# Optimization experiments

Hardware: AMD Instinct MI355X
Metric: run time of the kernel (lower is better)

## Reference

```python
import jax, jax.numpy as jnp
import numpy as np

FT = 0.2  # clip floor (init arg ft)

def _norm_mat(m):
    # matrix / (count of nonzeros along last dim + 1e-30)
    deg = jnp.sum(m != 0, axis=-1, keepdims=True).astype(m.dtype)
    return m / (deg + 1e-30)

def _l2n(x):
    return x / (jnp.linalg.norm(x, axis=-1, keepdims=True) + 1e-30)

def setup_inputs():
    B, L, D, H, O = 2, 2048, 64, 64, 128
    N = 2 * L
    ks = jax.random.split(jax.random.key(0), 30)
    u = lambda i, s: jax.random.uniform(ks[i], s, jnp.float32)
    g = lambda i, s: jax.random.normal(ks[i], s, jnp.float32) * 0.05
    inp = {}
    inp['word_outputs_0'] = g(0, (B, L, D))
    inp['word_outputs_1'] = g(1, (B, L, D))
    inp['node_hidden'] = g(2, (B, D))
    inp['op_embedding'] = g(3, (B, O, D))
    inp['word_exist_sequence'] = (u(4, (B, N)) < 0.8).astype(jnp.float32)
    inp['word_exist_matrix'] = (u(5, (B, N, N)) < 0.8).astype(jnp.float32)
    inp['word_operator'] = (u(6, (B, N, O)) < 0.02).astype(jnp.float32)
    inp['word_word'] = (u(7, (B, N, N)) < 0.01).astype(jnp.float32)
    inp['depend_0'] = (u(8, (B, L, L)) < 0.05).astype(jnp.float32)
    inp['depend_1'] = (u(9, (B, L, L)) < 0.05).astype(jnp.float32)
    inp['goal_word'] = u(10, (B, N))
    names = [('Wg', (D, H)), ('bg', (H,)), ('Wwk', (D, H)), ('bwk', (H,)),
             ('Wws', (D, H)), ('bws', (H,)), ('Wo', (D, D)), ('bo', (D,)),
             ('Wupd', (3 * H, D)), ('bupd', (D,)), ('Wf', (3 * H + D, D)), ('bf', (D,)),
             ('Wf2', (2 * D, D)), ('bf2', (D,)), ('Wout', (D, D)), ('bout', (D,))]
    for i, (nm, s) in enumerate(names):
        inp[nm] = g(11 + i, s)
    return inp

def _forward(w0, w1, nh, opE, wes, wem, wop, ww, d0, d1, gw,
             Wg, bg, Wwk, bwk, Wws, bws, Wo, bo, Wupd, bupd, Wf, bf, Wf2, bf2, Wout, bout):
    all_w = jnp.concatenate([w0, w1], axis=1)                      # [B,N,D]
    goal_trans = (nh @ Wg + bg)[:, None, :]                        # [B,1,H] (broadcast = expand)
    word_g = _l2n(goal_trans * gw[..., None])                      # [B,N,H]
    word_w_k = _l2n(jnp.matmul(_norm_mat(ww * wem), all_w @ Wwk + bwk))
    ws0 = jnp.matmul(_norm_mat(d0), w0 @ Wws + bws)
    ws1 = jnp.matmul(_norm_mat(d1), w1 @ Wws + bws)
    word_w_s = _l2n(jnp.concatenate([ws0, ws1], axis=1))           # [B,N,H]
    neigh = jnp.concatenate([word_g, word_w_k, word_w_s], axis=-1)  # [B,N,3H]
    forget = jax.nn.sigmoid(jnp.concatenate([all_w, word_g, word_w_k, word_w_s], axis=-1) @ Wf + bf)
    word_updated = jnp.maximum(forget, FT) * all_w + (1.0 - forget) * jax.nn.relu(neigh @ Wupd + bupd)
    adj_op = _norm_mat(jnp.swapaxes(wes[..., None] * wop, 1, 2))   # [B,O,N]
    word_op = jnp.matmul(adj_op, word_updated @ Wo + bo)           # [B,O,D]
    forget2 = jax.nn.sigmoid(jnp.concatenate([opE, word_op], axis=-1) @ Wf2 + bf2)
    op_out = jnp.maximum(forget2, FT) * opE + (1.0 - forget2) * jax.nn.relu(word_op @ Wout + bout)
    # original returns (split(word_updated), op_embedding); concat along node axis here
    return jnp.concatenate([word_updated, op_out], axis=1)         # [B,N+O,D]

def reference(word_outputs_0, word_outputs_1, node_hidden, op_embedding,
              word_exist_sequence, word_exist_matrix, word_operator, word_word,
              depend_0, depend_1, goal_word,
              Wg, bg, Wwk, bwk, Wws, bws, Wo, bo, Wupd, bupd, Wf, bf, Wf2, bf2, Wout, bout):
    return _forward(word_outputs_0, word_outputs_1, node_hidden, op_embedding,
                    word_exist_sequence, word_exist_matrix, word_operator, word_word,
                    depend_0, depend_1, goal_word,
                    Wg, bg, Wwk, bwk, Wws, bws, Wo, bo, Wupd, bupd, Wf, bf, Wf2, bf2, Wout, bout)
```

## Files before the change

### kernel.cpp

```cpp
#include <hip/hip_runtime.h>
#include <cstdint>

typedef unsigned short u16;
typedef unsigned long long u64;

__device__ __forceinline__ u16 f2b(float f){
  union { float f; uint32_t i; } v; v.f = f;
  uint32_t r = v.i + 0x7FFFu + ((v.i >> 16) & 1u);
  return (u16)(r >> 16);
}
__device__ __forceinline__ float b2f(u16 u){
  union { uint32_t i; float f; } v; v.i = ((uint32_t)u) << 16; return v.f;
}
__device__ __forceinline__ float sigmoidf(float x){ return 1.0f / (1.0f + __expf(-x)); }

__device__ __forceinline__ void gl_lds4(const void* g, void* l){
  __builtin_amdgcn_global_load_lds((const __attribute__((address_space(1))) void*)g,
                                   (__attribute__((address_space(3))) void*)l, 4, 0, 0);
}
#define WAIT_VM0() __builtin_amdgcn_s_waitcnt(0x0F70)

__global__ __launch_bounds__(256) void k_xform(
    const float* __restrict__ w0, const float* __restrict__ w1,
    const float* __restrict__ Wwk, const float* __restrict__ bwk,
    const float* __restrict__ Wws, const float* __restrict__ bws,
    const float* __restrict__ nh, const float* __restrict__ Wg, const float* __restrict__ bg,
    const float* __restrict__ Wf, const float* __restrict__ Wupd, const float* __restrict__ Wo,
    float* __restrict__ Xk, float* __restrict__ Xs,
    float* __restrict__ ghat, uint32_t* __restrict__ pkWf,
    uint32_t* __restrict__ pkWu, uint32_t* __restrict__ pkWo){
  int tid = threadIdx.x;
  if (blockIdx.x >= 512){
    int aux = blockIdx.x - 512;
    if (aux == 16){
      if (tid < 128){
        int b = tid >> 6, h = tid & 63;
        float g = bg[h];
        for (int d = 0; d < 64; ++d) g += nh[b*64 + d] * Wg[d*64 + h];
        float ss = g * g;
        #pragma unroll
        for (int o = 32; o > 0; o >>= 1) ss += __shfl_xor(ss, o, 64);
        ghat[b*64 + h] = g / (sqrtf(ss) + 1e-30f);
      }
      return;
    }
    for (int k = tid; k < 1024; k += 256){
      int i = aux*1024 + k;
      const float* src; uint32_t* dst; int li;
      if (i < 8192){ src = Wf; dst = pkWf; li = i; }
      else if (i < 14336){ src = Wupd; dst = pkWu; li = i - 8192; }
      else { src = Wo; dst = pkWo; li = i - 14336; }
      int k2 = li >> 6, ln = li & 63;
      dst[li] = (uint32_t)f2b(src[(2*k2)*64 + ln]) | ((uint32_t)f2b(src[(2*k2+1)*64 + ln]) << 16);
    }
    return;
  }
  __shared__ float sWk[4096], sWs[4096];
  for (int i = tid; i < 1024; i += 256){
    ((float4*)sWk)[i] = ((const float4*)Wwk)[i];
    ((float4*)sWs)[i] = ((const float4*)Wws)[i];
  }
  __syncthreads();
  int lane = tid & 63, wave = tid >> 6;
  float bk = bwk[lane], bs = bws[lane];
  float aw[4];
  #pragma unroll
  for (int t = 0; t < 4; ++t){
    int row = blockIdx.x*4 + wave + t*2048;
    int b = row >> 12, n = row & 4095;
    aw[t] = (n < 2048) ? w0[((size_t)(b*2048 + n))*64 + lane]
                       : w1[((size_t)(b*2048 + n - 2048))*64 + lane];
  }
  #pragma unroll
  for (int t = 0; t < 4; ++t){
    int row = blockIdx.x*4 + wave + t*2048;
    float xk = bk, xs = bs;
    #pragma unroll 8
    for (int d = 0; d < 64; ++d){
      float a = __shfl(aw[t], d, 64);
      xk += a * sWk[d*64 + lane];
      xs += a * sWs[d*64 + lane];
    }
    Xk[(size_t)row*64 + lane] = xk;
    Xs[(size_t)row*64 + lane] = xs;
  }
}

__global__ __launch_bounds__(256) void k_bits_all(
    const float* __restrict__ ww, const float* __restrict__ wem,
    const float* __restrict__ d0, const float* __restrict__ d1,
    const float* __restrict__ wes, const float* __restrict__ wop,
    u64* __restrict__ bitBig, u64* __restrict__ bitD0, u64* __restrict__ bitD1,
    u64* __restrict__ bitOp){
  int wid = blockIdx.x*4 + (threadIdx.x >> 6);
  int lane = threadIdx.x & 63;
  if (wid >= 49152){
    int ng0 = (wid - 49152) * 8;
    #pragma unroll
    for (int i = 0; i < 8; ++i){
      int n = ng0 + i;
      float vx = wop[(size_t)n*128 + lane];
      float vy = wop[(size_t)n*128 + 64 + lane];
      float e  = wes[n];
      u64 m0 = __ballot((e != 0.f) && (vx != 0.f));
      u64 m1 = __ballot((e != 0.f) && (vy != 0.f));
      if (lane == 0) bitOp[(size_t)n*2]     = m0;
      if (lane == 1) bitOp[(size_t)n*2 + 1] = m1;
    }
    return;
  }
  const float *A, *B; u64* dst;
  if (wid < 32768){
    A = ww + (size_t)wid*1024; B = wem + (size_t)wid*1024; dst = bitBig + (size_t)wid*16;
  } else if (wid < 40960){
    size_t c = wid - 32768; A = d0 + c*1024; B = A; dst = bitD0 + c*16;
  } else {
    size_t c = wid - 40960; A = d1 + c*1024; B = A; dst = bitD1 + c*16;
  }
  const float4* ap = (const float4*)A + lane;
  const float4* bp = (const float4*)B + lane;
  float4 a0 = ap[0], a1 = ap[64], a2 = ap[128], a3 = ap[192];
  float4 b0 = bp[0], b1 = bp[64], b2 = bp[128], b3 = bp[192];
  u64 myw = 0;
#define B4(i, va, vb) { \
  u64 m0 = __ballot((va.x != 0.f) && (vb.x != 0.f)); \
  u64 m1 = __ballot((va.y != 0.f) && (vb.y != 0.f)); \
  u64 m2 = __ballot((va.z != 0.f) && (vb.z != 0.f)); \
  u64 m3 = __ballot((va.w != 0.f) && (vb.w != 0.f)); \
  if (lane == (i)*4 + 0) myw = m0; \
  if (lane == (i)*4 + 1) myw = m1; \
  if (lane == (i)*4 + 2) myw = m2; \
  if (lane == (i)*4 + 3) myw = m3; }
  B4(0, a0, b0) B4(1, a1, b1) B4(2, a2, b2) B4(3, a3, b3)
#undef B4
  if (lane < 16) dst[lane] = myw;
}

__global__ __launch_bounds__(256) void k_gath_all(
    const u64* __restrict__ bitBig, const u64* __restrict__ bitD0, const u64* __restrict__ bitD1,
    const float* __restrict__ Xk, const float* __restrict__ Xs,
    u16* __restrict__ wwkn, u16* __restrict__ wwsn){
  __shared__ int q[4][256];
  __shared__ float rows[4][16][64];
  int lane = threadIdx.x & 63, wave = threadIdx.x >> 6;
  int wid = blockIdx.x*4 + wave;
  const u64* bits; const float* XbBase; u16* op; int WPR;
  if (wid < 8192){
    WPR = 64; bits = bitBig + (size_t)wid*64;
    int b = wid >> 12;
    XbBase = Xk + (size_t)b*4096*64;
    op = wwkn + (size_t)wid*64;
  } else if (wid < 12288){
    int lr = wid - 8192; WPR = 32; bits = bitD0 + (size_t)lr*32;
    int b = lr >> 11, r = lr & 2047;
    XbBase = Xs + (size_t)b*4096*64;
    op = wwsn + ((size_t)b*4096 + r)*64;
  } else {
    int lr = wid - 12288; WPR = 32; bits = bitD1 + (size_t)lr*32;
    int b = lr >> 11, r = lr & 2047;
    XbBase = Xs + ((size_t)b*4096 + 2048)*64;
    op = wwsn + ((size_t)b*4096 + 2048 + r)*64;
  }
  u64 word = (lane < WPR) ? bits[lane] : 0ULL;
  int c = __popcll(word);
  int pre = c;
  #pragma unroll
  for (int off = 1; off < 64; off <<= 1){
    int t = __shfl_up(pre, off, 64);
    if (lane >= off) pre += t;
  }
  int total = __shfl(pre, 63, 64);
  int base = pre - c;
  int colhi = (lane >> 2) * 256 + (lane & 3);
  u64 m = word;
  while (m){
    int p = __builtin_ctzll(m); m &= m - 1;
    q[wave][base++] = colhi + p*4;
  }
  float acc = 0.f;
  int i = 0;
  for (; i + 16 <= total; i += 16){
    int4 c0 = *(const int4*)&q[wave][i];
    int4 c1 = *(const int4*)&q[wave][i + 4];
    int4 c2 = *(const int4*)&q[wave][i + 8];
    int4 c3 = *(const int4*)&q[wave][i + 12];
    gl_lds4(XbBase + (size_t)c0.x*64 + lane, &rows[wave][ 0][0]);
    gl_lds4(XbBase + (size_t)c0.y*64 + lane, &rows[wave][ 1][0]);
    gl_lds4(XbBase + (size_t)c0.z*64 + lane, &rows[wave][ 2][0]);
    gl_lds4(XbBase + (size_t)c0.w*64 + lane, &rows[wave][ 3][0]);
    gl_lds4(XbBase + (size_t)c1.x*64 + lane, &rows[wave][ 4][0]);
    gl_lds4(XbBase + (size_t)c1.y*64 + lane, &rows[wave][ 5][0]);
    gl_lds4(XbBase + (size_t)c1.z*64 + lane, &rows[wave][ 6][0]);
    gl_lds4(XbBase + (size_t)c1.w*64 + lane, &rows[wave][ 7][0]);
    gl_lds4(XbBase + (size_t)c2.x*64 + lane, &rows[wave][ 8][0]);
    gl_lds4(XbBase + (size_t)c2.y*64 + lane, &rows[wave][ 9][0]);
    gl_lds4(XbBase + (size_t)c2.z*64 + lane, &rows[wave][10][0]);
    gl_lds4(XbBase + (size_t)c2.w*64 + lane, &rows[wave][11][0]);
    gl_lds4(XbBase + (size_t)c3.x*64 + lane, &rows[wave][12][0]);
    gl_lds4(XbBase + (size_t)c3.y*64 + lane, &rows[wave][13][0]);
    gl_lds4(XbBase + (size_t)c3.z*64 + lane, &rows[wave][14][0]);
    gl_lds4(XbBase + (size_t)c3.w*64 + lane, &rows[wave][15][0]);
    WAIT_VM0();
    float s0 = 0.f, s1 = 0.f, s2 = 0.f, s3 = 0.f;
    #pragma unroll
    for (int r = 0; r < 4; ++r){
      s0 += rows[wave][r][lane];
      s1 += rows[wave][4 + r][lane];
      s2 += rows[wave][8 + r][lane];
      s3 += rows[wave][12 + r][lane];
    }
    acc += (s0 + s1) + (s2 + s3);
  }
  for (; i < total; ++i) acc += XbBase[(size_t)q[wave][i]*64 + lane];
  float ss = acc * acc;
  #pragma unroll
  for (int o = 32; o > 0; o >>= 1) ss += __shfl_xor(ss, o, 64);
  op[lane] = f2b(acc / (sqrtf(ss) + 1e-30f));
}

__global__ __launch_bounds__(256, 2) void k_update(
    const float* __restrict__ w0, const float* __restrict__ w1,
    const float* __restrict__ gw, const float* __restrict__ ghat,
    const u16* __restrict__ wwkn, const u16* __restrict__ wwsn,
    const uint32_t* __restrict__ pkWf, const uint32_t* __restrict__ pkWu,
    const uint32_t* __restrict__ pkWo,
    const float* __restrict__ bf, const float* __restrict__ bupd, const float* __restrict__ bo,
    float* __restrict__ out, float* __restrict__ WUo){
  __shared__ uint32_t pWf[8192];
  __shared__ uint32_t pWu[6144];
  __shared__ uint32_t pWo[2048];
  __shared__ float xsh[4][256];
  int tid = threadIdx.x;
  for (int i = tid; i < 2048; i += 256) ((uint4*)pWf)[i] = ((const uint4*)pkWf)[i];
  for (int i = tid; i < 1536; i += 256) ((uint4*)pWu)[i] = ((const uint4*)pkWu)[i];
  for (int i = tid; i < 512;  i += 256) ((uint4*)pWo)[i] = ((const uint4*)pkWo)[i];
  __syncthreads();
  int lane = tid & 63, wave = tid >> 6;
  float bff = bf[lane], bup = bupd[lane], boo = bo[lane];
  float aw[4], wgv[4], wk[4], wsv[4];
  #pragma unroll
  for (int t = 0; t < 4; ++t){
    int row = blockIdx.x*4 + wave + t*2048;
    int b = row >> 12, n = row & 4095;
    aw[t] = (n < 2048) ? w0[((size_t)(b*2048 + n))*64 + lane]
                       : w1[((size_t)(b*2048 + n - 2048))*64 + lane];
    float gvv = gw[b*4096 + n];
    wgv[t] = (gvv != 0.f) ? ghat[b*64 + lane] : 0.f;
    wk[t]  = b2f(wwkn[(size_t)row*64 + lane]);
    wsv[t] = b2f(wwsn[(size_t)row*64 + lane]);
  }
  #pragma unroll
  for (int t = 0; t < 4; ++t){
    int row = blockIdx.x*4 + wave + t*2048;
    int b = row >> 12, n = row & 4095;
    xsh[wave][lane] = aw[t]; xsh[wave][64 + lane] = wgv[t];
    xsh[wave][128 + lane] = wk[t]; xsh[wave][192 + lane] = wsv[t];
    float f = bff, u = bup;
    #pragma unroll 8
    for (int k2 = 0; k2 < 32; ++k2){
      float2 xv = *(const float2*)&xsh[wave][2*k2];
      uint32_t wf = pWf[k2*64 + lane];
      f += xv.x * b2f((u16)wf) + xv.y * b2f((u16)(wf >> 16));
    }
    #pragma unroll 8
    for (int k2 = 32; k2 < 128; ++k2){
      float2 xv = *(const float2*)&xsh[wave][2*k2];
      uint32_t wf = pWf[k2*64 + lane];
      uint32_t wu = pWu[(k2 - 32)*64 + lane];
      f += xv.x * b2f((u16)wf) + xv.y * b2f((u16)(wf >> 16));
      u += xv.x * b2f((u16)wu) + xv.y * b2f((u16)(wu >> 16));
    }
    f = sigmoidf(f);
    u = fmaxf(u, 0.f);
    float wu = fmaxf(f, 0.2f) * aw[t] + (1.f - f) * u;
    out[((size_t)b*4224 + n)*64 + lane] = wu;
    float o = boo;
    #pragma unroll 8
    for (int k2 = 0; k2 < 32; ++k2){
      uint32_t wo2 = pWo[k2*64 + lane];
      o += __shfl(wu, 2*k2, 64) * b2f((u16)wo2) + __shfl(wu, 2*k2 + 1, 64) * b2f((u16)(wo2 >> 16));
    }
    WUo[(size_t)row*64 + lane] = o;
  }
}

__global__ __launch_bounds__(256) void k_opfin(
    const u64* __restrict__ bitOp, const float* __restrict__ WUo,
    const float* __restrict__ opE,
    const float* __restrict__ Wf2, const float* __restrict__ bf2,
    const float* __restrict__ Wout, const float* __restrict__ bout,
    float* __restrict__ out){
  __shared__ float sW2[8192];
  __shared__ float sWo[4096];
  __shared__ int q[4][96];
  __shared__ float sacc[4][64];
  __shared__ int scnt[4];
  __shared__ float xsh[128];
  int tid = threadIdx.x, lane = tid & 63, wave = tid >> 6;
  for (int i = tid; i < 2048; i += 256) ((float4*)sW2)[i] = ((const float4*)Wf2)[i];
  for (int i = tid; i < 1024; i += 256) ((float4*)sWo)[i] = ((const float4*)Wout)[i];
  int rowIdx = blockIdx.x;
  int b = rowIdx >> 7, o = rowIdx & 127;
  int wrd = o >> 6, bit = o & 63;
  const u64* bp = bitOp + (size_t)b*8192 + (size_t)wave*2048 + wrd;
  u64 lt = (1ULL << lane) - 1ULL;
  u64 vv[16];
  #pragma unroll
  for (int it = 0; it < 16; ++it) vv[it] = bp[(size_t)(it*64 + lane)*2];
  int cnt = 0;
  #pragma unroll
  for (int it = 0; it < 16; ++it){
    bool nz = (vv[it] >> bit) & 1ULL;
    u64 m = __ballot(nz);
    if (nz) q[wave][cnt + (int)__popcll(m & lt)] = wave*1024 + it*64 + lane;
    cnt += (int)__popcll(m);
  }
  const float* Xb = WUo + (size_t)b*4096*64 + lane;
  float acc = 0.f;
  int i = 0;
  for (; i + 8 <= cnt; i += 8){
    int4 c0 = *(const int4*)&q[wave][i];
    int4 c1 = *(const int4*)&q[wave][i + 4];
    float v0 = Xb[(size_t)c0.x*64], v1 = Xb[(size_t)c0.y*64];
    float v2 = Xb[(size_t)c0.z*64], v3 = Xb[(size_t)c0.w*64];
    float v4 = Xb[(size_t)c1.x*64], v5 = Xb[(size_t)c1.y*64];
    float v6 = Xb[(size_t)c1.z*64], v7 = Xb[(size_t)c1.w*64];
    acc += ((v0 + v1) + (v2 + v3)) + ((v4 + v5) + (v6 + v7));
  }
  for (; i < cnt; ++i) acc += Xb[(size_t)q[wave][i]*64];
  sacc[wave][lane] = acc;
  if (lane == 0) scnt[wave] = cnt;
  __syncthreads();
  if (wave == 0){
    float t = sacc[0][lane] + sacc[1][lane] + sacc[2][lane] + sacc[3][lane];
    float deg = (float)(scnt[0] + scnt[1] + scnt[2] + scnt[3]);
    float wo = t / (deg + 1e-30f);
    float e  = opE[(size_t)rowIdx*64 + lane];
    xsh[lane] = e; xsh[64 + lane] = wo;
    float f = bf2[lane], u = bout[lane];
    #pragma unroll 8
    for (int k = 0; k < 128; ++k) f += xsh[k] * sW2[k*64 + lane];
    #pragma unroll 8
    for (int d = 0; d < 64; ++d)  u += xsh[64 + d] * sWo[d*64 + lane];
    f = sigmoidf(f);
    u = fmaxf(u, 0.f);
    float res = fmaxf(f, 0.2f) * e + (1.f - f) * u;
    out[((size_t)b*4224 + 4096 + o)*64 + lane] = res;
  }
}

extern "C" void kernel_launch(void* const* d_in, const int* in_sizes, int n_in,
                              void* d_out, int out_size, void* d_ws, size_t ws_size,
                              hipStream_t stream){
  const float* w0   = (const float*)d_in[0];
  const float* w1   = (const float*)d_in[1];
  const float* nh   = (const float*)d_in[2];
  const float* opE  = (const float*)d_in[3];
  const float* wes  = (const float*)d_in[4];
  const float* wem  = (const float*)d_in[5];
  const float* wop  = (const float*)d_in[6];
  const float* ww   = (const float*)d_in[7];
  const float* d0   = (const float*)d_in[8];
  const float* d1   = (const float*)d_in[9];
  const float* gw   = (const float*)d_in[10];
  const float* Wg   = (const float*)d_in[11];
  const float* bg   = (const float*)d_in[12];
  const float* Wwk  = (const float*)d_in[13];
  const float* bwk  = (const float*)d_in[14];
  const float* Wws  = (const float*)d_in[15];
  const float* bws  = (const float*)d_in[16];
  const float* Wo   = (const float*)d_in[17];
  const float* bo   = (const float*)d_in[18];
  const float* Wupd = (const float*)d_in[19];
  const float* bupd = (const float*)d_in[20];
  const float* Wf   = (const float*)d_in[21];
  const float* bf   = (const float*)d_in[22];
  const float* Wf2  = (const float*)d_in[23];
  const float* bf2  = (const float*)d_in[24];
  const float* Wout = (const float*)d_in[25];
  const float* bout = (const float*)d_in[26];

  float* ws    = (float*)d_ws;
  float* ghat  = ws;
  float* Xk    = ws + 128;
  float* Xs    = ws + 524416;
  uint32_t* pkWf = (uint32_t*)(ws + 1048704);
  uint32_t* pkWu = (uint32_t*)(ws + 1056896);
  uint32_t* pkWo = (uint32_t*)(ws + 1063040);
  u64*  bitBig = (u64*)(ws + 1065088);
  u64*  bitD0  = (u64*)(ws + 2113664);
  u64*  bitD1  = (u64*)(ws + 2375808);
  u64*  bitOp  = (u64*)(ws + 2637952);
  u16*  wwkn   = (u16*)(ws + 2670720);
  u16*  wwsn   = (u16*)(ws + 2932864);
  float* WUo   = Xs;
  float* out   = (float*)d_out;

  k_xform<<<529, 256, 0, stream>>>(w0, w1, Wwk, bwk, Wws, bws, nh, Wg, bg,
                                   Wf, Wupd, Wo, Xk, Xs, ghat, pkWf, pkWu, pkWo);
  k_bits_all<<<12544, 256, 0, stream>>>(ww, wem, d0, d1, wes, wop,
                                        bitBig, bitD0, bitD1, bitOp);
  k_gath_all<<<4096, 256, 0, stream>>>(bitBig, bitD0, bitD1, Xk, Xs, wwkn, wwsn);
  k_update<<<512, 256, 0, stream>>>(w0, w1, gw, ghat, wwkn, wwsn,
                                    pkWf, pkWu, pkWo, bf, bupd, bo, out, WUo);
  k_opfin<<<256, 256, 0, stream>>>(bitOp, WUo, opE, Wf2, bf2, Wout, bout, out);
}
```

Baseline: 447.5 us.

## Aggregate raw word rows before linear projection and drop separate transform kernel

Uses linearity: instead of projecting every word through Wwk/Wws and then gathering projected rows, the gather kernel sums raw w0/w1 rows over each sparse neighbour set, then applies the 64x64 weight once per row, adding count times bias. This removes the k_xform kernel and its intermediate Xk/Xs buffers, and the weight packing and goal setup are folded into the bit-mask kernel as extra blocks. Each gather block now loads both weight matrices into LDS and does a per-row matvec after aggregation, which raises per-block LDS use and work; key and structural gathers run in one wave sequentially.

```diff
diff --git a/kernel.cpp b/kernel.cpp
--- a/kernel.cpp
+++ b/kernel.cpp
@@ -20,18 +20,18 @@
 }
 #define WAIT_VM0() __builtin_amdgcn_s_waitcnt(0x0F70)
 
-__global__ __launch_bounds__(256) void k_xform(
-    const float* __restrict__ w0, const float* __restrict__ w1,
-    const float* __restrict__ Wwk, const float* __restrict__ bwk,
-    const float* __restrict__ Wws, const float* __restrict__ bws,
+__global__ __launch_bounds__(256) void k_bits_all(
+    const float* __restrict__ ww, const float* __restrict__ wem,
+    const float* __restrict__ d0, const float* __restrict__ d1,
+    const float* __restrict__ wes, const float* __restrict__ wop,
     const float* __restrict__ nh, const float* __restrict__ Wg, const float* __restrict__ bg,
     const float* __restrict__ Wf, const float* __restrict__ Wupd, const float* __restrict__ Wo,
-    float* __restrict__ Xk, float* __restrict__ Xs,
-    float* __restrict__ ghat, uint32_t* __restrict__ pkWf,
-    uint32_t* __restrict__ pkWu, uint32_t* __restrict__ pkWo){
+    u64* __restrict__ bitBig, u64* __restrict__ bitD0, u64* __restrict__ bitD1,
+    u64* __restrict__ bitOp, float* __restrict__ ghat,
+    uint32_t* __restrict__ pkWf, uint32_t* __restrict__ pkWu, uint32_t* __restrict__ pkWo){
   int tid = threadIdx.x;
-  if (blockIdx.x >= 512){
-    int aux = blockIdx.x - 512;
+  if (blockIdx.x >= 12544){
+    int aux = blockIdx.x - 12544;
     if (aux == 16){
       if (tid < 128){
         int b = tid >> 6, h = tid & 63;
@@ -55,45 +55,8 @@
     }
     return;
   }
-  __shared__ float sWk[4096], sWs[4096];
-  for (int i = tid; i < 1024; i += 256){
-    ((float4*)sWk)[i] = ((const float4*)Wwk)[i];
-    ((float4*)sWs)[i] = ((const float4*)Wws)[i];
-  }
-  __syncthreads();
-  int lane = tid & 63, wave = tid >> 6;
-  float bk = bwk[lane], bs = bws[lane];
-  float aw[4];
-  #pragma unroll
-  for (int t = 0; t < 4; ++t){
-    int row = blockIdx.x*4 + wave + t*2048;
-    int b = row >> 12, n = row & 4095;
-    aw[t] = (n < 2048) ? w0[((size_t)(b*2048 + n))*64 + lane]
-                       : w1[((size_t)(b*2048 + n - 2048))*64 + lane];
-  }
-  #pragma unroll
-  for (int t = 0; t < 4; ++t){
-    int row = blockIdx.x*4 + wave + t*2048;
-    float xk = bk, xs = bs;
-    #pragma unroll 8
-    for (int d = 0; d < 64; ++d){
-      float a = __shfl(aw[t], d, 64);
-      xk += a * sWk[d*64 + lane];
-      xs += a * sWs[d*64 + lane];
-    }
-    Xk[(size_t)row*64 + lane] = xk;
-    Xs[(size_t)row*64 + lane] = xs;
-  }
-}
-
-__global__ __launch_bounds__(256) void k_bits_all(
-    const float* __restrict__ ww, const float* __restrict__ wem,
-    const float* __restrict__ d0, const float* __restrict__ d1,
-    const float* __restrict__ wes, const float* __restrict__ wop,
-    u64* __restrict__ bitBig, u64* __restrict__ bitD0, u64* __restrict__ bitD1,
-    u64* __restrict__ bitOp){
-  int wid = blockIdx.x*4 + (threadIdx.x >> 6);
-  int lane = threadIdx.x & 63;
+  int wid = blockIdx.x*4 + (tid >> 6);
+  int lane = tid & 63;
   if (wid >= 49152){
     int ng0 = (wid - 49152) * 8;
     #pragma unroll
@@ -136,86 +99,152 @@
   if (lane < 16) dst[lane] = myw;
 }
 
-__global__ __launch_bounds__(256) void k_gath_all(
+__global__ __launch_bounds__(256) void k_gath2(
     const u64* __restrict__ bitBig, const u64* __restrict__ bitD0, const u64* __restrict__ bitD1,
-    const float* __restrict__ Xk, const float* __restrict__ Xs,
+    const float* __restrict__ w0, const float* __restrict__ w1,
+    const float* __restrict__ Wwk, const float* __restrict__ bwk,
+    const float* __restrict__ Wws, const float* __restrict__ bws,
     u16* __restrict__ wwkn, u16* __restrict__ wwsn){
+  __shared__ float sWk[4096], sWs[4096];
   __shared__ int q[4][256];
   __shared__ float rows[4][16][64];
-  int lane = threadIdx.x & 63, wave = threadIdx.x >> 6;
+  int tid = threadIdx.x, lane = tid & 63, wave = tid >> 6;
+  for (int i = tid; i < 1024; i += 256){
+    ((float4*)sWk)[i] = ((const float4*)Wwk)[i];
+    ((float4*)sWs)[i] = ((const float4*)Wws)[i];
+  }
+  __syncthreads();
   int wid = blockIdx.x*4 + wave;
-  const u64* bits; const float* XbBase; u16* op; int WPR;
-  if (wid < 8192){
-    WPR = 64; bits = bitBig + (size_t)wid*64;
-    int b = wid >> 12;
-    XbBase = Xk + (size_t)b*4096*64;
-    op = wwkn + (size_t)wid*64;
-  } else if (wid < 12288){
-    int lr = wid - 8192; WPR = 32; bits = bitD0 + (size_t)lr*32;
-    int b = lr >> 11, r = lr & 2047;
-    XbBase = Xs + (size_t)b*4096*64;
-    op = wwsn + ((size_t)b*4096 + r)*64;
-  } else {
-    int lr = wid - 12288; WPR = 32; bits = bitD1 + (size_t)lr*32;
-    int b = lr >> 11, r = lr & 2047;
-    XbBase = Xs + ((size_t)b*4096 + 2048)*64;
-    op = wwsn + ((size_t)b*4096 + 2048 + r)*64;
-  }
-  u64 word = (lane < WPR) ? bits[lane] : 0ULL;
-  int c = __popcll(word);
-  int pre = c;
-  #pragma unroll
-  for (int off = 1; off < 64; off <<= 1){
-    int t = __shfl_up(pre, off, 64);
-    if (lane >= off) pre += t;
-  }
-  int total = __shfl(pre, 63, 64);
-  int base = pre - c;
-  int colhi = (lane >> 2) * 256 + (lane & 3);
-  u64 m = word;
-  while (m){
-    int p = __builtin_ctzll(m); m &= m - 1;
-    q[wave][base++] = colhi + p*4;
-  }
-  float acc = 0.f;
-  int i = 0;
-  for (; i + 16 <= total; i += 16){
-    int4 c0 = *(const int4*)&q[wave][i];
-    int4 c1 = *(const int4*)&q[wave][i + 4];
-    int4 c2 = *(const int4*)&q[wave][i + 8];
-    int4 c3 = *(const int4*)&q[wave][i + 12];
-    gl_lds4(XbBase + (size_t)c0.x*64 + lane, &rows[wave][ 0][0]);
-    gl_lds4(XbBase + (size_t)c0.y*64 + lane, &rows[wave][ 1][0]);
-    gl_lds4(XbBase + (size_t)c0.z*64 + lane, &rows[wave][ 2][0]);
-    gl_lds4(XbBase + (size_t)c0.w*64 + lane, &rows[wave][ 3][0]);
-    gl_lds4(XbBase + (size_t)c1.x*64 + lane, &rows[wave][ 4][0]);
-    gl_lds4(XbBase + (size_t)c1.y*64 + lane, &rows[wave][ 5][0]);
-    gl_lds4(XbBase + (size_t)c1.z*64 + lane, &rows[wave][ 6][0]);
-    gl_lds4(XbBase + (size_t)c1.w*64 + lane, &rows[wave][ 7][0]);
-    gl_lds4(XbBase + (size_t)c2.x*64 + lane, &rows[wave][ 8][0]);
-    gl_lds4(XbBase + (size_t)c2.y*64 + lane, &rows[wave][ 9][0]);
-    gl_lds4(XbBase + (size_t)c2.z*64 + lane, &rows[wave][10][0]);
-    gl_lds4(XbBase + (size_t)c2.w*64 + lane, &rows[wave][11][0]);
-    gl_lds4(XbBase + (size_t)c3.x*64 + lane, &rows[wave][12][0]);
-    gl_lds4(XbBase + (size_t)c3.y*64 + lane, &rows[wave][13][0]);
-    gl_lds4(XbBase + (size_t)c3.z*64 + lane, &rows[wave][14][0]);
-    gl_lds4(XbBase + (size_t)c3.w*64 + lane, &rows[wave][15][0]);
-    WAIT_VM0();
-    float s0 = 0.f, s1 = 0.f, s2 = 0.f, s3 = 0.f;
+  int b = wid >> 12, n = wid & 4095;
+  const float* w0b = w0 + (size_t)b*131072 + lane;
+  const float* w1b = w1 + (size_t)b*131072 - 131072 + lane;
+
+  {
+    u64 word = bitBig[(size_t)wid*64 + lane];
+    int c = __popcll(word);
+    int pre = c;
     #pragma unroll
-    for (int r = 0; r < 4; ++r){
-      s0 += rows[wave][r][lane];
-      s1 += rows[wave][4 + r][lane];
-      s2 += rows[wave][8 + r][lane];
-      s3 += rows[wave][12 + r][lane];
-    }
-    acc += (s0 + s1) + (s2 + s3);
-  }
-  for (; i < total; ++i) acc += XbBase[(size_t)q[wave][i]*64 + lane];
-  float ss = acc * acc;
-  #pragma unroll
-  for (int o = 32; o > 0; o >>= 1) ss += __shfl_xor(ss, o, 64);
-  op[lane] = f2b(acc / (sqrtf(ss) + 1e-30f));
+    for (int off = 1; off < 64; off <<= 1){
+      int t = __shfl_up(pre, off, 64);
+      if (lane >= off) pre += t;
+    }
+    int total = __shfl(pre, 63, 64);
+    int base = pre - c;
+    int colhi = (lane >> 2) * 256 + (lane & 3);
+    u64 m = word;
+    while (m){
+      int p = __builtin_ctzll(m); m &= m - 1;
+      q[wave][base++] = colhi + p*4;
+    }
+#define GP(j) ((((j) < 2048) ? w0b : w1b) + (size_t)(j)*64)
+    float acc = 0.f;
+    int i = 0;
+    for (; i + 16 <= total; i += 16){
+      int4 c0 = *(const int4*)&q[wave][i];
+      int4 c1 = *(const int4*)&q[wave][i + 4];
+      int4 c2 = *(const int4*)&q[wave][i + 8];
+      int4 c3 = *(const int4*)&q[wave][i + 12];
+      gl_lds4(GP(c0.x), &rows[wave][ 0][0]);
+      gl_lds4(GP(c0.y), &rows[wave][ 1][0]);
+      gl_lds4(GP(c0.z), &rows[wave][ 2][0]);
+      gl_lds4(GP(c0.w), &rows[wave][ 3][0]);
+      gl_lds4(GP(c1.x), &rows[wave][ 4][0]);
+      gl_lds4(GP(c1.y), &rows[wave][ 5][0]);
+      gl_lds4(GP(c1.z), &rows[wave][ 6][0]);
+      gl_lds4(GP(c1.w), &rows[wave][ 7][0]);
+      gl_lds4(GP(c2.x), &rows[wave][ 8][0]);
+      gl_lds4(GP(c2.y), &rows[wave][ 9][0]);
+      gl_lds4(GP(c2.z), &rows[wave][10][0]);
+      gl_lds4(GP(c2.w), &rows[wave][11][0]);
+      gl_lds4(GP(c3.x), &rows[wave][12][0]);
+      gl_lds4(GP(c3.y), &rows[wave][13][0]);
+      gl_lds4(GP(c3.z), &rows[wave][14][0]);
+      gl_lds4(GP(c3.w), &rows[wave][15][0]);
+      WAIT_VM0();
+      float s0 = 0.f, s1 = 0.f, s2 = 0.f, s3 = 0.f;
+      #pragma unroll
+      for (int r = 0; r < 4; ++r){
+        s0 += rows[wave][r][lane];
+        s1 += rows[wave][4 + r][lane];
+        s2 += rows[wave][8 + r][lane];
+        s3 += rows[wave][12 + r][lane];
+      }
+      acc += (s0 + s1) + (s2 + s3);
+    }
+    for (; i < total; ++i) acc += *GP(q[wave][i]);
+#undef GP
+    float y = (float)total * bwk[lane];
+    #pragma unroll 8
+    for (int d = 0; d < 64; ++d) y += __shfl(acc, d, 64) * sWk[d*64 + lane];
+    float ss = y * y;
+    #pragma unroll
+    for (int o = 32; o > 0; o >>= 1) ss += __shfl_xor(ss, o, 64);
+    wwkn[(size_t)wid*64 + lane] = f2b(y / (sqrtf(ss) + 1e-30f));
+  }
+
+  {
+    const u64* bits = (n < 2048) ? (bitD0 + ((size_t)b*2048 + n)*32)
+                                 : (bitD1 + ((size_t)b*2048 + n - 2048)*32);
+    const float* src = ((n < 2048) ? w0 : w1) + (size_t)b*131072 + lane;
+    u64 word = (lane < 32) ? bits[lane] : 0ULL;
+    int c = __popcll(word);
+    int pre = c;
+    #pragma unroll
+    for (int off = 1; off < 64; off <<= 1){
+      int t = __shfl_up(pre, off, 64);
+      if (lane >= off) pre += t;
+    }
+    int total = __shfl(pre, 63, 64);
+    int base = pre - c;
+    int colhi = (lane >> 2) * 256 + (lane & 3);
+    u64 m = word;
+    while (m){
+      int p = __builtin_ctzll(m); m &= m - 1;
+      q[wave][base++] = colhi + p*4;
+    }
+    float acc = 0.f;
+    int i = 0;
+    for (; i + 16 <= total; i += 16){
+      int4 c0 = *(const int4*)&q[wave][i];
+      int4 c1 = *(const int4*)&q[wave][i + 4];
+      int4 c2 = *(const int4*)&q[wave][i + 8];
+      int4 c3 = *(const int4*)&q[wave][i + 12];
+      gl_lds4(src + (size_t)c0.x*64, &rows[wave][ 0][0]);
+      gl_lds4(src + (size_t)c0.y*64, &rows[wave][ 1][0]);
+      gl_lds4(src + (size_t)c0.z*64, &rows[wave][ 2][0]);
+      gl_lds4(src + (size_t)c0.w*64, &rows[wave][ 3][0]);
+      gl_lds4(src + (size_t)c1.x*64, &rows[wave][ 4][0]);
+      gl_lds4(src + (size_t)c1.y*64, &rows[wave][ 5][0]);
+      gl_lds4(src + (size_t)c1.z*64, &rows[wave][ 6][0]);
+      gl_lds4(src + (size_t)c1.w*64, &rows[wave][ 7][0]);
+      gl_lds4(src + (size_t)c2.x*64, &rows[wave][ 8][0]);
+      gl_lds4(src + (size_t)c2.y*64, &rows[wave][ 9][0]);
+      gl_lds4(src + (size_t)c2.z*64, &rows[wave][10][0]);
+      gl_lds4(src + (size_t)c2.w*64, &rows[wave][11][0]);
+      gl_lds4(src + (size_t)c3.x*64, &rows[wave][12][0]);
+      gl_lds4(src + (size_t)c3.y*64, &rows[wave][13][0]);
+      gl_lds4(src + (size_t)c3.z*64, &rows[wave][14][0]);
+      gl_lds4(src + (size_t)c3.w*64, &rows[wave][15][0]);
+      WAIT_VM0();
+      float s0 = 0.f, s1 = 0.f, s2 = 0.f, s3 = 0.f;
+      #pragma unroll
+      for (int r = 0; r < 4; ++r){
+        s0 += rows[wave][r][lane];
+        s1 += rows[wave][4 + r][lane];
+        s2 += rows[wave][8 + r][lane];
+        s3 += rows[wave][12 + r][lane];
+      }
+      acc += (s0 + s1) + (s2 + s3);
+    }
+    for (; i < total; ++i) acc += src[(size_t)q[wave][i]*64];
+    float y = (float)total * bws[lane];
+    #pragma unroll 8
+    for (int d = 0; d < 64; ++d) y += __shfl(acc, d, 64) * sWs[d*64 + lane];
+    float ss = y * y;
+    #pragma unroll
+    for (int o = 32; o > 0; o >>= 1) ss += __shfl_xor(ss, o, 64);
+    wwsn[(size_t)wid*64 + lane] = f2b(y / (sqrtf(ss) + 1e-30f));
+  }
 }
 
 __global__ __launch_bounds__(256, 2) void k_update(
@@ -382,25 +411,23 @@
 
   float* ws    = (float*)d_ws;
   float* ghat  = ws;
-  float* Xk    = ws + 128;
-  float* Xs    = ws + 524416;
-  uint32_t* pkWf = (uint32_t*)(ws + 1048704);
-  uint32_t* pkWu = (uint32_t*)(ws + 1056896);
-  uint32_t* pkWo = (uint32_t*)(ws + 1063040);
-  u64*  bitBig = (u64*)(ws + 1065088);
-  u64*  bitD0  = (u64*)(ws + 2113664);
-  u64*  bitD1  = (u64*)(ws + 2375808);
-  u64*  bitOp  = (u64*)(ws + 2637952);
-  u16*  wwkn   = (u16*)(ws + 2670720);
-  u16*  wwsn   = (u16*)(ws + 2932864);
-  float* WUo   = Xs;
+  uint32_t* pkWf = (uint32_t*)(ws + 128);
+  uint32_t* pkWu = (uint32_t*)(ws + 8320);
+  uint32_t* pkWo = (uint32_t*)(ws + 14464);
+  u64*  bitBig = (u64*)(ws + 16512);
+  u64*  bitD0  = (u64*)(ws + 1065088);
+  u64*  bitD1  = (u64*)(ws + 1327232);
+  u64*  bitOp  = (u64*)(ws + 1589376);
+  u16*  wwkn   = (u16*)(ws + 1622144);
+  u16*  wwsn   = (u16*)(ws + 1884288);
+  float* WUo   = ws + 2146432;
   float* out   = (float*)d_out;
 
-  k_xform<<<529, 256, 0, stream>>>(w0, w1, Wwk, bwk, Wws, bws, nh, Wg, bg,
-                                   Wf, Wupd, Wo, Xk, Xs, ghat, pkWf, pkWu, pkWo);
-  k_bits_all<<<12544, 256, 0, stream>>>(ww, wem, d0, d1, wes, wop,
-                                        bitBig, bitD0, bitD1, bitOp);
-  k_gath_all<<<4096, 256, 0, stream>>>(bitBig, bitD0, bitD1, Xk, Xs, wwkn, wwsn);
+  k_bits_all<<<12561, 256, 0, stream>>>(ww, wem, d0, d1, wes, wop, nh, Wg, bg,
+                                        Wf, Wupd, Wo, bitBig, bitD0, bitD1,
+                                        bitOp, ghat, pkWf, pkWu, pkWo);
+  k_gath2<<<2048, 256, 0, stream>>>(bitBig, bitD0, bitD1, w0, w1,
+                                    Wwk, bwk, Wws, bws, wwkn, wwsn);
   k_update<<<512, 256, 0, stream>>>(w0, w1, gw, ghat, wwkn, wwsn,
                                     pkWf, pkWu, pkWo, bf, bupd, bo, out, WUo);
   k_opfin<<<256, 256, 0, stream>>>(bitOp, WUo, opE, Wf2, bf2, Wout, bout, out);
```

New measurement: 456.7 us. +2.1%, slower.

## Reassociate sparse aggregation to gather raw inputs, apply projection after summing

Applied to the files above, without the earlier changes.

The sparse-adjacency matmul is reordered so each wave builds its nonzero mask and immediately gathers raw w0/w1 rows, producing per-chunk partial sums and counts. The dense Wwk/Wws projection and bias are applied afterwards in a new finishing kernel as S@W + count*b. This removes the separate transform kernel, the bitmask round-trip through memory and one launch. In exchange, partial sums are stored in bf16, which adds rounding before the projection, and row gathers are split across chunks.

```diff
diff --git a/kernel.cpp b/kernel.cpp
--- a/kernel.cpp
+++ b/kernel.cpp
@@ -20,18 +20,22 @@
 }
 #define WAIT_VM0() __builtin_amdgcn_s_waitcnt(0x0F70)
 
-__global__ __launch_bounds__(256) void k_xform(
+__global__ __launch_bounds__(256) void k_bits_all(
+    const float* __restrict__ ww, const float* __restrict__ wem,
+    const float* __restrict__ d0, const float* __restrict__ d1,
+    const float* __restrict__ wes, const float* __restrict__ wop,
     const float* __restrict__ w0, const float* __restrict__ w1,
-    const float* __restrict__ Wwk, const float* __restrict__ bwk,
-    const float* __restrict__ Wws, const float* __restrict__ bws,
     const float* __restrict__ nh, const float* __restrict__ Wg, const float* __restrict__ bg,
     const float* __restrict__ Wf, const float* __restrict__ Wupd, const float* __restrict__ Wo,
-    float* __restrict__ Xk, float* __restrict__ Xs,
-    float* __restrict__ ghat, uint32_t* __restrict__ pkWf,
-    uint32_t* __restrict__ pkWu, uint32_t* __restrict__ pkWo){
+    u16* __restrict__ psumB, int* __restrict__ pcntB,
+    u16* __restrict__ psumD, int* __restrict__ pcntD,
+    u64* __restrict__ bitOp, float* __restrict__ ghat,
+    uint32_t* __restrict__ pkWf, uint32_t* __restrict__ pkWu, uint32_t* __restrict__ pkWo){
+  __shared__ int q[4][256];
+  __shared__ float rows[4][16][64];
   int tid = threadIdx.x;
-  if (blockIdx.x >= 512){
-    int aux = blockIdx.x - 512;
+  if (blockIdx.x >= 12544){
+    int aux = blockIdx.x - 12544;
     if (aux == 16){
       if (tid < 128){
         int b = tid >> 6, h = tid & 63;
@@ -55,45 +59,8 @@
     }
     return;
   }
-  __shared__ float sWk[4096], sWs[4096];
-  for (int i = tid; i < 1024; i += 256){
-    ((float4*)sWk)[i] = ((const float4*)Wwk)[i];
-    ((float4*)sWs)[i] = ((const float4*)Wws)[i];
-  }
-  __syncthreads();
-  int lane = tid & 63, wave = tid >> 6;
-  float bk = bwk[lane], bs = bws[lane];
-  float aw[4];
-  #pragma unroll
-  for (int t = 0; t < 4; ++t){
-    int row = blockIdx.x*4 + wave + t*2048;
-    int b = row >> 12, n = row & 4095;
-    aw[t] = (n < 2048) ? w0[((size_t)(b*2048 + n))*64 + lane]
-                       : w1[((size_t)(b*2048 + n - 2048))*64 + lane];
-  }
-  #pragma unroll
-  for (int t = 0; t < 4; ++t){
-    int row = blockIdx.x*4 + wave + t*2048;
-    float xk = bk, xs = bs;
-    #pragma unroll 8
-    for (int d = 0; d < 64; ++d){
-      float a = __shfl(aw[t], d, 64);
-      xk += a * sWk[d*64 + lane];
-      xs += a * sWs[d*64 + lane];
-    }
-    Xk[(size_t)row*64 + lane] = xk;
-    Xs[(size_t)row*64 + lane] = xs;
-  }
-}
-
-__global__ __launch_bounds__(256) void k_bits_all(
-    const float* __restrict__ ww, const float* __restrict__ wem,
-    const float* __restrict__ d0, const float* __restrict__ d1,
-    const float* __restrict__ wes, const float* __restrict__ wop,
-    u64* __restrict__ bitBig, u64* __restrict__ bitD0, u64* __restrict__ bitD1,
-    u64* __restrict__ bitOp){
-  int wid = blockIdx.x*4 + (threadIdx.x >> 6);
-  int lane = threadIdx.x & 63;
+  int wave = tid >> 6, lane = tid & 63;
+  int wid = blockIdx.x*4 + wave;
   if (wid >= 49152){
     int ng0 = (wid - 49152) * 8;
     #pragma unroll
@@ -109,13 +76,34 @@
     }
     return;
   }
-  const float *A, *B; u64* dst;
+  const float *A, *B;
+  const float *srcA, *srcB;
+  int jbase, thresh;
+  u16* ps; int* pc;
   if (wid < 32768){
-    A = ww + (size_t)wid*1024; B = wem + (size_t)wid*1024; dst = bitBig + (size_t)wid*16;
-  } else if (wid < 40960){
-    size_t c = wid - 32768; A = d0 + c*1024; B = A; dst = bitD0 + c*16;
+    int row = wid >> 2, chunk = wid & 3;
+    int b = row >> 12;
+    A = ww  + (size_t)row*4096 + chunk*1024;
+    B = wem + (size_t)row*4096 + chunk*1024;
+    srcA = w0 + (size_t)b*131072 + lane;
+    srcB = w1 + (size_t)b*131072 - 131072 + lane;
+    jbase = chunk*1024; thresh = 2048;
+    ps = psumB + (size_t)wid*64; pc = pcntB + wid;
   } else {
-    size_t c = wid - 40960; A = d1 + c*1024; B = A; dst = bitD1 + c*16;
+    int idx = wid - 32768;
+    int rowp = idx >> 1, chunk = idx & 1;
+    if (rowp < 4096){
+      int b = rowp >> 11;
+      A = d0 + (size_t)rowp*2048 + chunk*1024;
+      srcA = w0 + (size_t)b*131072 + lane;
+    } else {
+      int rr = rowp - 4096, b = rr >> 11;
+      A = d1 + (size_t)rr*2048 + chunk*1024;
+      srcA = w1 + (size_t)b*131072 + lane;
+    }
+    B = A; srcB = srcA;
+    jbase = chunk*1024; thresh = 4096;
+    ps = psumD + (size_t)idx*64; pc = pcntD + idx;
   }
   const float4* ap = (const float4*)A + lane;
   const float4* bp = (const float4*)B + lane;
@@ -133,36 +121,7 @@
   if (lane == (i)*4 + 3) myw = m3; }
   B4(0, a0, b0) B4(1, a1, b1) B4(2, a2, b2) B4(3, a3, b3)
 #undef B4
-  if (lane < 16) dst[lane] = myw;
-}
-
-__global__ __launch_bounds__(256) void k_gath_all(
-    const u64* __restrict__ bitBig, const u64* __restrict__ bitD0, const u64* __restrict__ bitD1,
-    const float* __restrict__ Xk, const float* __restrict__ Xs,
-    u16* __restrict__ wwkn, u16* __restrict__ wwsn){
-  __shared__ int q[4][256];
-  __shared__ float rows[4][16][64];
-  int lane = threadIdx.x & 63, wave = threadIdx.x >> 6;
-  int wid = blockIdx.x*4 + wave;
-  const u64* bits; const float* XbBase; u16* op; int WPR;
-  if (wid < 8192){
-    WPR = 64; bits = bitBig + (size_t)wid*64;
-    int b = wid >> 12;
-    XbBase = Xk + (size_t)b*4096*64;
-    op = wwkn + (size_t)wid*64;
-  } else if (wid < 12288){
-    int lr = wid - 8192; WPR = 32; bits = bitD0 + (size_t)lr*32;
-    int b = lr >> 11, r = lr & 2047;
-    XbBase = Xs + (size_t)b*4096*64;
-    op = wwsn + ((size_t)b*4096 + r)*64;
-  } else {
-    int lr = wid - 12288; WPR = 32; bits = bitD1 + (size_t)lr*32;
-    int b = lr >> 11, r = lr & 2047;
-    XbBase = Xs + ((size_t)b*4096 + 2048)*64;
-    op = wwsn + ((size_t)b*4096 + 2048 + r)*64;
-  }
-  u64 word = (lane < WPR) ? bits[lane] : 0ULL;
-  int c = __popcll(word);
+  int c = __popcll(myw);
   int pre = c;
   #pragma unroll
   for (int off = 1; off < 64; off <<= 1){
@@ -172,11 +131,12 @@
   int total = __shfl(pre, 63, 64);
   int base = pre - c;
   int colhi = (lane >> 2) * 256 + (lane & 3);
-  u64 m = word;
+  u64 m = myw;
   while (m){
     int p = __builtin_ctzll(m); m &= m - 1;
     q[wave][base++] = colhi + p*4;
   }
+#define GPJ(qv) (((jbase + (qv)) < thresh ? srcA : srcB) + (size_t)(jbase + (qv))*64)
   float acc = 0.f;
   int i = 0;
   for (; i + 16 <= total; i += 16){
@@ -184,22 +144,22 @@
     int4 c1 = *(const int4*)&q[wave][i + 4];
     int4 c2 = *(const int4*)&q[wave][i + 8];
     int4 c3 = *(const int4*)&q[wave][i + 12];
-    gl_lds4(XbBase + (size_t)c0.x*64 + lane, &rows[wave][ 0][0]);
-    gl_lds4(XbBase + (size_t)c0.y*64 + lane, &rows[wave][ 1][0]);
-    gl_lds4(XbBase + (size_t)c0.z*64 + lane, &rows[wave][ 2][0]);
-    gl_lds4(XbBase + (size_t)c0.w*64 + lane, &rows[wave][ 3][0]);
-    gl_lds4(XbBase + (size_t)c1.x*64 + lane, &rows[wave][ 4][0]);
-    gl_lds4(XbBase + (size_t)c1.y*64 + lane, &rows[wave][ 5][0]);
-    gl_lds4(XbBase + (size_t)c1.z*64 + lane, &rows[wave][ 6][0]);
-    gl_lds4(XbBase + (size_t)c1.w*64 + lane, &rows[wave][ 7][0]);
-    gl_lds4(XbBase + (size_t)c2.x*64 + lane, &rows[wave][ 8][0]);
-    gl_lds4(XbBase + (size_t)c2.y*64 + lane, &rows[wave][ 9][0]);
-    gl_lds4(XbBase + (size_t)c2.z*64 + lane, &rows[wave][10][0]);
-    gl_lds4(XbBase + (size_t)c2.w*64 + lane, &rows[wave][11][0]);
-    gl_lds4(XbBase + (size_t)c3.x*64 + lane, &rows[wave][12][0]);
-    gl_lds4(XbBase + (size_t)c3.y*64 + lane, &rows[wave][13][0]);
-    gl_lds4(XbBase + (size_t)c3.z*64 + lane, &rows[wave][14][0]);
-    gl_lds4(XbBase + (size_t)c3.w*64 + lane, &rows[wave][15][0]);
+    gl_lds4(GPJ(c0.x), &rows[wave][ 0][0]);
+    gl_lds4(GPJ(c0.y), &rows[wave][ 1][0]);
+    gl_lds4(GPJ(c0.z), &rows[wave][ 2][0]);
+    gl_lds4(GPJ(c0.w), &rows[wave][ 3][0]);
+    gl_lds4(GPJ(c1.x), &rows[wave][ 4][0]);
+    gl_lds4(GPJ(c1.y), &rows[wave][ 5][0]);
+    gl_lds4(GPJ(c1.z), &rows[wave][ 6][0]);
+    gl_lds4(GPJ(c1.w), &rows[wave][ 7][0]);
+    gl_lds4(GPJ(c2.x), &rows[wave][ 8][0]);
+    gl_lds4(GPJ(c2.y), &rows[wave][ 9][0]);
+    gl_lds4(GPJ(c2.z), &rows[wave][10][0]);
+    gl_lds4(GPJ(c2.w), &rows[wave][11][0]);
+    gl_lds4(GPJ(c3.x), &rows[wave][12][0]);
+    gl_lds4(GPJ(c3.y), &rows[wave][13][0]);
+    gl_lds4(GPJ(c3.z), &rows[wave][14][0]);
+    gl_lds4(GPJ(c3.w), &rows[wave][15][0]);
     WAIT_VM0();
     float s0 = 0.f, s1 = 0.f, s2 = 0.f, s3 = 0.f;
     #pragma unroll
@@ -211,11 +171,48 @@
     }
     acc += (s0 + s1) + (s2 + s3);
   }
-  for (; i < total; ++i) acc += XbBase[(size_t)q[wave][i]*64 + lane];
-  float ss = acc * acc;
+  for (; i < total; ++i) acc += *GPJ(q[wave][i]);
+#undef GPJ
+  ps[lane] = f2b(acc);
+  if (lane == 0) pc[0] = total;
+}
+
+__global__ __launch_bounds__(256) void k_fin(
+    const u16* __restrict__ psumB, const int* __restrict__ pcntB,
+    const u16* __restrict__ psumD, const int* __restrict__ pcntD,
+    const float* __restrict__ Wwk, const float* __restrict__ bwk,
+    const float* __restrict__ Wws, const float* __restrict__ bws,
+    u16* __restrict__ wwkn, u16* __restrict__ wwsn){
+  __shared__ float sWk[4096], sWs[4096];
+  int tid = threadIdx.x, lane = tid & 63, wave = tid >> 6;
+  for (int i = tid; i < 1024; i += 256){
+    ((float4*)sWk)[i] = ((const float4*)Wwk)[i];
+    ((float4*)sWs)[i] = ((const float4*)Wws)[i];
+  }
+  __syncthreads();
+  int wid = blockIdx.x*4 + wave;
+  float S; float y; const float* sW; u16* outp; size_t oidx;
+  if (wid < 8192){
+    S = b2f(psumB[((size_t)wid*4 + 0)*64 + lane]) + b2f(psumB[((size_t)wid*4 + 1)*64 + lane])
+      + b2f(psumB[((size_t)wid*4 + 2)*64 + lane]) + b2f(psumB[((size_t)wid*4 + 3)*64 + lane]);
+    int T = pcntB[wid*4] + pcntB[wid*4 + 1] + pcntB[wid*4 + 2] + pcntB[wid*4 + 3];
+    y = (float)T * bwk[lane]; sW = sWk; outp = wwkn; oidx = wid;
+  } else {
+    int rp = wid - 8192;
+    S = b2f(psumD[((size_t)rp*2 + 0)*64 + lane]) + b2f(psumD[((size_t)rp*2 + 1)*64 + lane]);
+    int T = pcntD[rp*2] + pcntD[rp*2 + 1];
+    y = (float)T * bws[lane]; sW = sWs; outp = wwsn;
+    int b, n;
+    if (rp < 4096){ b = rp >> 11; n = rp & 2047; }
+    else { int rr = rp - 4096; b = rr >> 11; n = 2048 + (rr & 2047); }
+    oidx = (size_t)b*4096 + n;
+  }
+  #pragma unroll 8
+  for (int d = 0; d < 64; ++d) y += __shfl(S, d, 64) * sW[d*64 + lane];
+  float ss = y * y;
   #pragma unroll
   for (int o = 32; o > 0; o >>= 1) ss += __shfl_xor(ss, o, 64);
-  op[lane] = f2b(acc / (sqrtf(ss) + 1e-30f));
+  outp[oidx*64 + lane] = f2b(y / (sqrtf(ss) + 1e-30f));
 }
 
 __global__ __launch_bounds__(256, 2) void k_update(
@@ -382,25 +379,25 @@
 
   float* ws    = (float*)d_ws;
   float* ghat  = ws;
-  float* Xk    = ws + 128;
-  float* Xs    = ws + 524416;
-  uint32_t* pkWf = (uint32_t*)(ws + 1048704);
-  uint32_t* pkWu = (uint32_t*)(ws + 1056896);
-  uint32_t* pkWo = (uint32_t*)(ws + 1063040);
-  u64*  bitBig = (u64*)(ws + 1065088);
-  u64*  bitD0  = (u64*)(ws + 2113664);
-  u64*  bitD1  = (u64*)(ws + 2375808);
-  u64*  bitOp  = (u64*)(ws + 2637952);
-  u16*  wwkn   = (u16*)(ws + 2670720);
-  u16*  wwsn   = (u16*)(ws + 2932864);
-  float* WUo   = Xs;
+  uint32_t* pkWf = (uint32_t*)(ws + 128);
+  uint32_t* pkWu = (uint32_t*)(ws + 8320);
+  uint32_t* pkWo = (uint32_t*)(ws + 14464);
+  u64*  bitOp  = (u64*)(ws + 16512);
+  u16*  psumB  = (u16*)(ws + 49280);
+  int*  pcntB  = (int*)(ws + 1097856);
+  u16*  psumD  = (u16*)(ws + 1130624);
+  int*  pcntD  = (int*)(ws + 1654912);
+  u16*  wwkn   = (u16*)(ws + 1671296);
+  u16*  wwsn   = (u16*)(ws + 1933440);
+  float* WUo   = ws + 2195584;
   float* out   = (float*)d_out;
 
-  k_xform<<<529, 256, 0, stream>>>(w0, w1, Wwk, bwk, Wws, bws, nh, Wg, bg,
-                                   Wf, Wupd, Wo, Xk, Xs, ghat, pkWf, pkWu, pkWo);
-  k_bits_all<<<12544, 256, 0, stream>>>(ww, wem, d0, d1, wes, wop,
-                                        bitBig, bitD0, bitD1, bitOp);
-  k_gath_all<<<4096, 256, 0, stream>>>(bitBig, bitD0, bitD1, Xk, Xs, wwkn, wwsn);
+  k_bits_all<<<12561, 256, 0, stream>>>(ww, wem, d0, d1, wes, wop, w0, w1,
+                                        nh, Wg, bg, Wf, Wupd, Wo,
+                                        psumB, pcntB, psumD, pcntD,
+                                        bitOp, ghat, pkWf, pkWu, pkWo);
+  k_fin<<<4096, 256, 0, stream>>>(psumB, pcntB, psumD, pcntD,
+                                  Wwk, bwk, Wws, bws, wwkn, wwsn);
   k_update<<<512, 256, 0, stream>>>(w0, w1, gw, ghat, wwkn, wwsn,
                                     pkWf, pkWu, pkWo, bf, bupd, bo, out, WUo);
   k_opfin<<<256, 256, 0, stream>>>(bitOp, WUo, opE, Wf2, bf2, Wout, bout, out);
```

After: 443.2 us. No clear change (-1.0%).
